# Performance work log

Hardware: AMD Instinct MI355X
Metric: run time of the kernel (lower is better)

## Reference

```python
import jax, jax.numpy as jnp
import numpy as np

NUM_EMBEDDINGS = 1024
EMBEDDING_DIM = 256
COMMITMENT_COST = 0.5
DECAY = 0.99
EPS = 1e-5


def setup_inputs() -> dict:
    key = jax.random.key(0)
    k1, k2, k3 = jax.random.split(key, 3)
    B, K, D = 64, 512, EMBEDDING_DIM
    return {
        "z_e": jax.random.normal(k1, (B, K, D), dtype=jnp.float32),
        "codebook": jax.random.normal(k2, (NUM_EMBEDDINGS, D), dtype=jnp.float32),
        "ema_cluster_size": jnp.ones((NUM_EMBEDDINGS,), dtype=jnp.float32),
        "ema_embed_sum": jax.random.normal(k3, (NUM_EMBEDDINGS, D), dtype=jnp.float32),
    }


def reference(z_e, codebook, ema_cluster_size, ema_embed_sum):
    B, K, D = z_e.shape
    flat = z_e.reshape(-1, D)  # [N, D]
    z_sq = jnp.sum(flat * flat, axis=1, keepdims=True)          # [N, 1]
    c_sq = jnp.sum(codebook * codebook, axis=1)[None, :]        # [1, E]
    distances = z_sq + c_sq - 2.0 * flat @ codebook.T           # [N, E]
    indices = jnp.argmin(distances, axis=1)                     # [N]
    z_q_flat = codebook[indices]                                # [N, D] gather (old codebook)

    # EMA statistics (training path), via segment sums instead of dense one-hot
    batch_cluster_size = jax.ops.segment_sum(
        jnp.ones_like(indices, dtype=flat.dtype), indices, num_segments=NUM_EMBEDDINGS)
    batch_embed_sum = jax.ops.segment_sum(flat, indices, num_segments=NUM_EMBEDDINGS)
    new_cluster_size = DECAY * ema_cluster_size + (1.0 - DECAY) * batch_cluster_size
    new_embed_sum = DECAY * ema_embed_sum + (1.0 - DECAY) * batch_embed_sum
    n = jnp.sum(new_cluster_size)
    smoothed = (new_cluster_size + EPS) / (n + NUM_EMBEDDINGS * EPS) * n
    new_codebook = new_embed_sum / smoothed[:, None]

    z_q = z_q_flat.reshape(B, K, D)
    commitment_loss = jnp.mean((z_e - jax.lax.stop_gradient(z_q)) ** 2)
    vq_loss = COMMITMENT_COST * commitment_loss
    # straight-through estimator
    z_q = z_e + jax.lax.stop_gradient(z_q - z_e)
    return z_q, vq_loss, indices.reshape(B, K), new_codebook, new_cluster_size, new_embed_sum
```

## Files before the change

kernel.cpp:

```cpp
#include <hip/hip_runtime.h>

typedef unsigned long long u64;
typedef unsigned int u32;
typedef __attribute__((ext_vector_type(8))) short short8;
typedef __attribute__((ext_vector_type(4))) float f32x4;

#define N_ROWS 32768
#define DIM    256
#define NE     1024

#define O_ZQ   0
#define O_LOSS 8388608
#define O_IDX  8388609
#define O_NCB  8421377
#define O_NCS  8683521
#define O_NES  8684545

#define OFF_LOSS   0
#define OFF_N      1
#define OFF_CSQ    64
#define OFF_CNT    1088
#define OFF_FILL   2112
#define OFF_BASE   3200
#define OFF_IDX    4224
#define OFF_BUCKET 36992
#define OFF_KEY    69888
#define OFF_CB16   135424

#define MARGIN   2.0f
#define LIST_CAP 3072

__device__ __forceinline__ unsigned short bf16rne(float x) {
    u32 b = __float_as_uint(x);
    return (unsigned short)((b + 0x7FFFu + ((b >> 16) & 1u)) >> 16);
}

__global__ __launch_bounds__(256) void prep_kernel(const float* __restrict__ cb,
                                                   float* __restrict__ ws,
                                                   float* __restrict__ out_nes) {
    const int tid = threadIdx.x, b = blockIdx.x;
    const int g = b * 256 + tid;

#pragma unroll
    for (int j = 0; j < 4; ++j) out_nes[g + j * 65536] = 0.f;
    if (g < N_ROWS) ((u64*)(ws + OFF_KEY))[g] = ~0ull;
    if (g < 2048) ws[OFF_CNT + g] = 0.f;
    if (g == 0) ws[OFF_LOSS] = 0.f;

    const int e = b * 4 + (tid >> 6);
    const int lane = tid & 63;
    float4 v = *(const float4*)(cb + (size_t)e * DIM + lane * 4);
    ushort4 h;
    h.x = bf16rne(v.x); h.y = bf16rne(v.y); h.z = bf16rne(v.z); h.w = bf16rne(v.w);
    *(ushort4*)((unsigned short*)(ws + OFF_CB16) + (size_t)e * DIM + lane * 4) = h;
    float s = v.x * v.x + v.y * v.y + v.z * v.z + v.w * v.w;
#pragma unroll
    for (int off = 32; off >= 1; off >>= 1) s += __shfl_down(s, off, 64);
    if (lane == 0) ws[OFF_CSQ + e] = s;
}

__global__ __launch_bounds__(512, 2) void vq_main(const float* __restrict__ z,
                                                  const float* __restrict__ cb,
                                                  float* __restrict__ ws,
                                                  float* __restrict__ out_zq,
                                                  float* __restrict__ out_idx) {
    __shared__ unsigned short zs[128][256];
    __shared__ unsigned short cbs[256][128];
    __shared__ float csq_s[NE];
    __shared__ u32   list[LIST_CAP];
    __shared__ int   lcnt;
    __shared__ int   sidx[128];
    __shared__ float lred[8];

    const int tid  = threadIdx.x;
    const int row0 = blockIdx.x * 128;
    const unsigned short* cb16 = (const unsigned short*)(ws + OFF_CB16);
    u64* keys = (u64*)(ws + OFF_KEY);

    if (tid == 0) lcnt = 0;
    csq_s[tid]       = ws[OFF_CSQ + tid];
    csq_s[tid + 512] = ws[OFF_CSQ + tid + 512];

#pragma unroll
    for (int sweep = 0; sweep < 8; ++sweep) {
        int fi = sweep * 4096 + tid * 8;
        int r = fi >> 8, c = fi & 255;
        const float4* src = (const float4*)(z + (size_t)row0 * DIM + fi);
        float4 v0 = src[0], v1 = src[1];
        short8 p;
        p[0] = (short)bf16rne(v0.x); p[1] = (short)bf16rne(v0.y);
        p[2] = (short)bf16rne(v0.z); p[3] = (short)bf16rne(v0.w);
        p[4] = (short)bf16rne(v1.x); p[5] = (short)bf16rne(v1.y);
        p[6] = (short)bf16rne(v1.z); p[7] = (short)bf16rne(v1.w);
        *(short8*)&zs[r][c ^ (8 * (r & 15))] = p;
    }

    const int wid = tid >> 6, lane = tid & 63;
    const int wm = wid >> 2, wn = wid & 3;
    const int l15 = lane & 15, l4 = lane >> 4;
    const int arow_base = wm * 64;
    const int swz = 8 * l15;

    float runmin[4][4];
#pragma unroll
    for (int m = 0; m < 4; ++m)
#pragma unroll
        for (int rg = 0; rg < 4; ++rg) runmin[m][rg] = 3.4e38f;

    for (int chunk = 0; chunk < 4; ++chunk) {
        const int e0 = chunk * 256;
        f32x4 acc[4][4];
#pragma unroll
        for (int m = 0; m < 4; ++m)
#pragma unroll
            for (int n = 0; n < 4; ++n) acc[m][n] = (f32x4){0.f, 0.f, 0.f, 0.f};

        for (int kh = 0; kh < 2; ++kh) {
            __syncthreads();
#pragma unroll
            for (int sweep = 0; sweep < 8; ++sweep) {
                int r  = sweep * 32 + (tid >> 4);
                int lk = (tid & 15) * 8;
                short8 v = *(const short8*)(cb16 + (size_t)(e0 + r) * DIM + kh * 128 + lk);
                *(short8*)&cbs[r][lk ^ (8 * (r & 15))] = v;
            }
            __syncthreads();
#pragma unroll
            for (int ks = 0; ks < 4; ++ks) {
                short8 a[4], bfr[4];
                int acol = kh * 128 + ks * 32 + 8 * l4;
                int bcol = ks * 32 + 8 * l4;
#pragma unroll
                for (int m = 0; m < 4; ++m)
                    a[m] = *(const short8*)&zs[arow_base + m * 16 + l15][acol ^ swz];
#pragma unroll
                for (int n = 0; n < 4; ++n)
                    bfr[n] = *(const short8*)&cbs[wn * 64 + n * 16 + l15][bcol ^ swz];
#pragma unroll
                for (int m = 0; m < 4; ++m)
#pragma unroll
                    for (int n = 0; n < 4; ++n)
                        acc[m][n] = __builtin_amdgcn_mfma_f32_16x16x32_bf16(
                            a[m], bfr[n], acc[m][n], 0, 0, 0);
            }
        }
        float cq[4];
#pragma unroll
        for (int n = 0; n < 4; ++n) cq[n] = csq_s[e0 + wn * 64 + n * 16 + l15];
#pragma unroll
        for (int m = 0; m < 4; ++m) {
#pragma unroll
            for (int rg = 0; rg < 4; ++rg) {
                float cmin = 3.4e38f;
#pragma unroll
                for (int n = 0; n < 4; ++n)
                    cmin = fminf(cmin, fmaf(-2.0f, acc[m][n][rg], cq[n]));
#pragma unroll
                for (int off = 1; off <= 8; off <<= 1)
                    cmin = fminf(cmin, __shfl_xor(cmin, off, 16));
                runmin[m][rg] = fminf(runmin[m][rg], cmin);
                float thr = runmin[m][rg] + MARGIN;
                int lrow = arow_base + m * 16 + l4 * 4 + rg;
#pragma unroll
                for (int n = 0; n < 4; ++n) {
                    float d = fmaf(-2.0f, acc[m][n][rg], cq[n]);
                    if (d <= thr) {
                        int slot = atomicAdd(&lcnt, 1);
                        if (slot < LIST_CAP)
                            list[slot] = ((u32)lrow << 10) |
                                         (u32)(e0 + wn * 64 + n * 16 + l15);
                    }
                }
            }
        }
    }
    __syncthreads();

    int nlist = lcnt < LIST_CAP ? lcnt : LIST_CAP;
    const int grp = tid >> 4, gl = tid & 15;
    for (int i = grp; i < nlist; i += 32) {
        u32 ent = list[i];
        int lrow = ent >> 10, code = ent & 1023;
        const float* zr = z + (size_t)(row0 + lrow) * DIM + gl * 16;
        const float* cr = cb + (size_t)code * DIM + gl * 16;
        float s = 0.f;
#pragma unroll
        for (int j = 0; j < 4; ++j) {
            float4 zv = ((const float4*)zr)[j];
            float4 cv = ((const float4*)cr)[j];
            s = fmaf(zv.x, cv.x, s); s = fmaf(zv.y, cv.y, s);
            s = fmaf(zv.z, cv.z, s); s = fmaf(zv.w, cv.w, s);
        }
#pragma unroll
        for (int off = 1; off <= 8; off <<= 1) s += __shfl_xor(s, off, 16);
        if (gl == 0) {
            float d = fmaf(-2.0f, s, csq_s[code]);
            u32 bb = __float_as_uint(d);
            u32 mm = (bb & 0x80000000u) ? ~bb : (bb | 0x80000000u);
            u64 key = ((u64)mm << 10) | (u32)code;
            atomicMin(&keys[row0 + lrow], key);
        }
    }
    __syncthreads();

    if (tid < 128) {
        u64 key = atomicMin(&keys[row0 + tid], ~0ull);
        int idx = (int)(key & 1023u);
        sidx[tid] = idx;
        out_idx[row0 + tid] = (float)idx;
        ((int*)ws)[OFF_IDX + row0 + tid] = idx;
        atomicAdd(&ws[OFF_CNT + idx], 1.0f);
    }
    __syncthreads();

    float lsum = 0.f;
    {
        int r = tid >> 2, part = tid & 3;
        int e = sidx[r];
        const float4* crow = (const float4*)(cb + (size_t)e * DIM + part * 64);
        const float4* zrow = (const float4*)(z + (size_t)(row0 + r) * DIM + part * 64);
        float4*       qrow = (float4*)(out_zq + (size_t)(row0 + r) * DIM + part * 64);
#pragma unroll
        for (int j = 0; j < 16; ++j) {
            float4 c4 = crow[j];
            float4 z4 = zrow[j];
            qrow[j] = c4;
            float dx = z4.x - c4.x, dy = z4.y - c4.y;
            float dz = z4.z - c4.z, dw = z4.w - c4.w;
            lsum += dx * dx + dy * dy + dz * dz + dw * dw;
        }
    }
#pragma unroll
    for (int off = 32; off >= 1; off >>= 1) lsum += __shfl_down(lsum, off, 64);
    if ((tid & 63) == 0) lred[tid >> 6] = lsum;
    __syncthreads();
    if (tid == 0) {
        float t = 0.f;
#pragma unroll
        for (int w = 0; w < 8; ++w) t += lred[w];
        atomicAdd(&ws[OFF_LOSS], t);
    }
}

__global__ __launch_bounds__(1024) void finalize_a(const float* __restrict__ ema_cs,
                                                   float* __restrict__ ws,
                                                   float* __restrict__ out_ncs,
                                                   float* __restrict__ out_loss) {
    __shared__ float wred[16];
    __shared__ int   wscan[16];
    const int tid = threadIdx.x, lane = tid & 63, w = tid >> 6;

    float cnt = ws[OFF_CNT + tid];
    float ncs = 0.99f * ema_cs[tid] + 0.01f * cnt;
    out_ncs[tid] = ncs;

    float s = ncs;
#pragma unroll
    for (int off = 32; off >= 1; off >>= 1) s += __shfl_down(s, off, 64);

    int v = (int)cnt;
    int x = v;
#pragma unroll
    for (int off = 1; off < 64; off <<= 1) {
        int o = __shfl_up(x, off, 64);
        if (lane >= off) x += o;
    }
    if (lane == 63) wscan[w] = x;
    if (lane == 0)  wred[w]  = s;
    __syncthreads();
    if (tid == 0) {
        float n = 0.f;
#pragma unroll
        for (int k = 0; k < 16; ++k) n += wred[k];
        ws[OFF_N] = n;
        out_loss[0] = 0.5f * ws[OFF_LOSS] / 8388608.0f;
        int run = 0;
#pragma unroll
        for (int k = 0; k < 16; ++k) { int t = wscan[k]; wscan[k] = run; run += t; }
    }
    __syncthreads();
    ((int*)ws)[OFF_BASE + tid] = x - v + wscan[w];
}

__global__ __launch_bounds__(256) void scatter_rows(float* __restrict__ ws) {
    int row = blockIdx.x * 256 + threadIdx.x;
    int* wsi = (int*)ws;
    int e = wsi[OFF_IDX + row];
    int slot = atomicAdd(&wsi[OFF_FILL + e], 1);
    wsi[OFF_BUCKET + wsi[OFF_BASE + e] + slot] = row;
}

__global__ __launch_bounds__(256) void seg_reduce(const float* __restrict__ z,
                                                  const float* __restrict__ ws,
                                                  float* __restrict__ bsum) {
    __shared__ int srow[32];
    __shared__ int scode[32];
    const int tid = threadIdx.x;
    const int p0  = blockIdx.x * 32;
    const int* wsi = (const int*)ws;

    if (tid < 32) {
        int row = wsi[OFF_BUCKET + p0 + tid];
        srow[tid]  = row;
        scode[tid] = wsi[OFF_IDX + row];
    }
    __syncthreads();

    const int d = tid;
    float acc = 0.f;
    int prev = scode[0];
#pragma unroll 4
    for (int i = 0; i < 32; ++i) {
        int e = scode[i];
        if (e != prev) {
            atomicAdd(&bsum[(size_t)prev * DIM + d], acc);
            acc = 0.f;
            prev = e;
        }
        acc += z[(size_t)srow[i] * DIM + d];
    }
    atomicAdd(&bsum[(size_t)prev * DIM + d], acc);
}

__global__ __launch_bounds__(256) void finalize_b(const float* __restrict__ ema_sum,
                                                  const float* __restrict__ ws,
                                                  const float* __restrict__ out_ncs,
                                                  float* __restrict__ out_nes,
                                                  float* __restrict__ out_ncb) {
    const int e = blockIdx.x, d = threadIdx.x;
    const size_t i = (size_t)e * DIM + d;
    float bsum = out_nes[i];
    float nes  = 0.99f * ema_sum[i] + 0.01f * bsum;
    out_nes[i] = nes;
    float ncs = out_ncs[e];
    float n   = ws[OFF_N];
    float sm  = (ncs + 1e-5f) / (n + NE * 1e-5f) * n;
    out_ncb[i] = nes / sm;
}

extern "C" void kernel_launch(void* const* d_in, const int* in_sizes, int n_in,
                              void* d_out, int out_size, void* d_ws, size_t ws_size,
                              hipStream_t stream) {
    const float* z_e      = (const float*)d_in[0];
    const float* codebook = (const float*)d_in[1];
    const float* ema_cs   = (const float*)d_in[2];
    const float* ema_sum  = (const float*)d_in[3];
    float* out = (float*)d_out;
    float* ws  = (float*)d_ws;

    prep_kernel<<<256, 256, 0, stream>>>(codebook, ws, out + O_NES);

    vq_main<<<256, 512, 0, stream>>>(z_e, codebook, ws, out + O_ZQ, out + O_IDX);

    finalize_a<<<1, 1024, 0, stream>>>(ema_cs, ws, out + O_NCS, out + O_LOSS);

    scatter_rows<<<N_ROWS / 256, 256, 0, stream>>>(ws);

    seg_reduce<<<N_ROWS / 32, 256, 0, stream>>>(z_e, ws, out + O_NES);

    finalize_b<<<NE, 256, 0, stream>>>(ema_sum, ws, out + O_NCS,
                                       out + O_NES, out + O_NCB);
}
```

Before: 228.5 us.

## Prefetch codebook tiles, compute loss from distances, fuse post-processing into cooperative kernel

Several changes land at once. In the main VQ kernel, the next codebook tile is prefetched into registers while the current tile is being multiplied, and the refinement dot products now use 4 lanes per candidate instead of 16. The commitment loss is derived from the winning distance plus a per-row ||z||^2 computed during staging, which removes the reread of z and codebook. The z_q write, finalize_a, scatter, segment reduce and finalize_b are merged into one cooperative kernel with grid syncs, which removes several launches at the cost of grid-wide barriers and register pressure from the prefetch. Deriving the loss from distances also changes its numerics slightly, since it is clamped at zero.

```diff
diff --git a/kernel.cpp b/kernel.cpp
--- a/kernel.cpp
+++ b/kernel.cpp
@@ -1,4 +1,7 @@
 #include <hip/hip_runtime.h>
+#include <hip/hip_cooperative_groups.h>
+
+namespace cg = cooperative_groups;
 
 typedef unsigned long long u64;
 typedef unsigned int u32;
@@ -62,24 +65,33 @@
 __global__ __launch_bounds__(512, 2) void vq_main(const float* __restrict__ z,
                                                   const float* __restrict__ cb,
                                                   float* __restrict__ ws,
-                                                  float* __restrict__ out_zq,
                                                   float* __restrict__ out_idx) {
     __shared__ unsigned short zs[128][256];
     __shared__ unsigned short cbs[256][128];
     __shared__ float csq_s[NE];
     __shared__ u32   list[LIST_CAP];
     __shared__ int   lcnt;
-    __shared__ int   sidx[128];
+    __shared__ float zsq_s[128];
     __shared__ float lred[8];
 
     const int tid  = threadIdx.x;
     const int row0 = blockIdx.x * 128;
     const unsigned short* cb16 = (const unsigned short*)(ws + OFF_CB16);
     u64* keys = (u64*)(ws + OFF_KEY);
+    int* wsi  = (int*)ws;
+
+    const int sr_c = tid >> 4;
+    const int lk_c = (tid & 15) * 8;
+    short8 stg[8];
+#pragma unroll
+    for (int s = 0; s < 8; ++s)
+        stg[s] = *(const short8*)(cb16 + (size_t)(s * 32 + sr_c) * DIM + lk_c);
 
     if (tid == 0) lcnt = 0;
+    if (tid < 128) zsq_s[tid] = 0.f;
     csq_s[tid]       = ws[OFF_CSQ + tid];
     csq_s[tid + 512] = ws[OFF_CSQ + tid + 512];
+    __syncthreads();
 
 #pragma unroll
     for (int sweep = 0; sweep < 8; ++sweep) {
@@ -93,6 +105,9 @@
         p[4] = (short)bf16rne(v1.x); p[5] = (short)bf16rne(v1.y);
         p[6] = (short)bf16rne(v1.z); p[7] = (short)bf16rne(v1.w);
         *(short8*)&zs[r][c ^ (8 * (r & 15))] = p;
+        float sq = v0.x * v0.x + v0.y * v0.y + v0.z * v0.z + v0.w * v0.w
+                 + v1.x * v1.x + v1.y * v1.y + v1.z * v1.z + v1.w * v1.w;
+        atomicAdd(&zsq_s[r], sq);
     }
 
     const int wid = tid >> 6, lane = tid & 63;
@@ -107,68 +122,77 @@
 #pragma unroll
         for (int rg = 0; rg < 4; ++rg) runmin[m][rg] = 3.4e38f;
 
-    for (int chunk = 0; chunk < 4; ++chunk) {
-        const int e0 = chunk * 256;
-        f32x4 acc[4][4];
-#pragma unroll
-        for (int m = 0; m < 4; ++m)
-#pragma unroll
-            for (int n = 0; n < 4; ++n) acc[m][n] = (f32x4){0.f, 0.f, 0.f, 0.f};
-
-        for (int kh = 0; kh < 2; ++kh) {
-            __syncthreads();
-#pragma unroll
-            for (int sweep = 0; sweep < 8; ++sweep) {
-                int r  = sweep * 32 + (tid >> 4);
-                int lk = (tid & 15) * 8;
-                short8 v = *(const short8*)(cb16 + (size_t)(e0 + r) * DIM + kh * 128 + lk);
-                *(short8*)&cbs[r][lk ^ (8 * (r & 15))] = v;
-            }
-            __syncthreads();
-#pragma unroll
-            for (int ks = 0; ks < 4; ++ks) {
-                short8 a[4], bfr[4];
-                int acol = kh * 128 + ks * 32 + 8 * l4;
-                int bcol = ks * 32 + 8 * l4;
-#pragma unroll
-                for (int m = 0; m < 4; ++m)
-                    a[m] = *(const short8*)&zs[arow_base + m * 16 + l15][acol ^ swz];
+    f32x4 acc[4][4];
+
+    for (int phase = 0; phase < 8; ++phase) {
+        const int chunk = phase >> 1, kh = phase & 1;
+        const int e0 = chunk << 8;
+        if (kh == 0) {
+#pragma unroll
+            for (int m = 0; m < 4; ++m)
+#pragma unroll
+                for (int n = 0; n < 4; ++n) acc[m][n] = (f32x4){0.f, 0.f, 0.f, 0.f};
+        }
+        __syncthreads();
+#pragma unroll
+        for (int s = 0; s < 8; ++s) {
+            int r = s * 32 + sr_c;
+            *(short8*)&cbs[r][lk_c ^ (8 * (r & 15))] = stg[s];
+        }
+        __syncthreads();
+        if (phase < 7) {
+            int np = phase + 1;
+            int nbase = (np >> 1) * 256, nkh = np & 1;
+#pragma unroll
+            for (int s = 0; s < 8; ++s)
+                stg[s] = *(const short8*)(cb16 + (size_t)(nbase + s * 32 + sr_c) * DIM
+                                          + nkh * 128 + lk_c);
+        }
+#pragma unroll
+        for (int ks = 0; ks < 4; ++ks) {
+            short8 a[4], bfr[4];
+            int acol = kh * 128 + ks * 32 + 8 * l4;
+            int bcol = ks * 32 + 8 * l4;
+#pragma unroll
+            for (int m = 0; m < 4; ++m)
+                a[m] = *(const short8*)&zs[arow_base + m * 16 + l15][acol ^ swz];
+#pragma unroll
+            for (int n = 0; n < 4; ++n)
+                bfr[n] = *(const short8*)&cbs[wn * 64 + n * 16 + l15][bcol ^ swz];
+#pragma unroll
+            for (int m = 0; m < 4; ++m)
 #pragma unroll
                 for (int n = 0; n < 4; ++n)
-                    bfr[n] = *(const short8*)&cbs[wn * 64 + n * 16 + l15][bcol ^ swz];
-#pragma unroll
-                for (int m = 0; m < 4; ++m)
+                    acc[m][n] = __builtin_amdgcn_mfma_f32_16x16x32_bf16(
+                        a[m], bfr[n], acc[m][n], 0, 0, 0);
+        }
+        if (kh == 1) {
+            float cq[4];
+#pragma unroll
+            for (int n = 0; n < 4; ++n) cq[n] = csq_s[e0 + wn * 64 + n * 16 + l15];
+#pragma unroll
+            for (int m = 0; m < 4; ++m) {
+#pragma unroll
+                for (int rg = 0; rg < 4; ++rg) {
+                    float cmin = 3.4e38f;
 #pragma unroll
                     for (int n = 0; n < 4; ++n)
-                        acc[m][n] = __builtin_amdgcn_mfma_f32_16x16x32_bf16(
-                            a[m], bfr[n], acc[m][n], 0, 0, 0);
-            }
-        }
-        float cq[4];
-#pragma unroll
-        for (int n = 0; n < 4; ++n) cq[n] = csq_s[e0 + wn * 64 + n * 16 + l15];
-#pragma unroll
-        for (int m = 0; m < 4; ++m) {
-#pragma unroll
-            for (int rg = 0; rg < 4; ++rg) {
-                float cmin = 3.4e38f;
-#pragma unroll
-                for (int n = 0; n < 4; ++n)
-                    cmin = fminf(cmin, fmaf(-2.0f, acc[m][n][rg], cq[n]));
-#pragma unroll
-                for (int off = 1; off <= 8; off <<= 1)
-                    cmin = fminf(cmin, __shfl_xor(cmin, off, 16));
-                runmin[m][rg] = fminf(runmin[m][rg], cmin);
-                float thr = runmin[m][rg] + MARGIN;
-                int lrow = arow_base + m * 16 + l4 * 4 + rg;
-#pragma unroll
-                for (int n = 0; n < 4; ++n) {
-                    float d = fmaf(-2.0f, acc[m][n][rg], cq[n]);
-                    if (d <= thr) {
-                        int slot = atomicAdd(&lcnt, 1);
-                        if (slot < LIST_CAP)
-                            list[slot] = ((u32)lrow << 10) |
-                                         (u32)(e0 + wn * 64 + n * 16 + l15);
+                        cmin = fminf(cmin, fmaf(-2.0f, acc[m][n][rg], cq[n]));
+#pragma unroll
+                    for (int off = 1; off <= 8; off <<= 1)
+                        cmin = fminf(cmin, __shfl_xor(cmin, off, 16));
+                    runmin[m][rg] = fminf(runmin[m][rg], cmin);
+                    float thr = runmin[m][rg] + MARGIN;
+                    int lrow = arow_base + m * 16 + l4 * 4 + rg;
+#pragma unroll
+                    for (int n = 0; n < 4; ++n) {
+                        float d = fmaf(-2.0f, acc[m][n][rg], cq[n]);
+                        if (d <= thr) {
+                            int slot = atomicAdd(&lcnt, 1);
+                            if (slot < LIST_CAP)
+                                list[slot] = ((u32)lrow << 10) |
+                                             (u32)(e0 + wn * 64 + n * 16 + l15);
+                        }
                     }
                 }
             }
@@ -177,22 +201,22 @@
     __syncthreads();
 
     int nlist = lcnt < LIST_CAP ? lcnt : LIST_CAP;
-    const int grp = tid >> 4, gl = tid & 15;
-    for (int i = grp; i < nlist; i += 32) {
+    const int grp = tid >> 2, gl = tid & 3;
+    for (int i = grp; i < nlist; i += 128) {
         u32 ent = list[i];
         int lrow = ent >> 10, code = ent & 1023;
-        const float* zr = z + (size_t)(row0 + lrow) * DIM + gl * 16;
-        const float* cr = cb + (size_t)code * DIM + gl * 16;
+        const float4* zr = (const float4*)(z + (size_t)(row0 + lrow) * DIM);
+        const float4* cr = (const float4*)(cb + (size_t)code * DIM);
         float s = 0.f;
 #pragma unroll
-        for (int j = 0; j < 4; ++j) {
-            float4 zv = ((const float4*)zr)[j];
-            float4 cv = ((const float4*)cr)[j];
+        for (int j = 0; j < 16; ++j) {
+            float4 zv = zr[j * 4 + gl];
+            float4 cv = cr[j * 4 + gl];
             s = fmaf(zv.x, cv.x, s); s = fmaf(zv.y, cv.y, s);
             s = fmaf(zv.z, cv.z, s); s = fmaf(zv.w, cv.w, s);
         }
-#pragma unroll
-        for (int off = 1; off <= 8; off <<= 1) s += __shfl_xor(s, off, 16);
+        s += __shfl_xor(s, 1, 4);
+        s += __shfl_xor(s, 2, 4);
         if (gl == 0) {
             float d = fmaf(-2.0f, s, csq_s[code]);
             u32 bb = __float_as_uint(d);
@@ -203,32 +227,17 @@
     }
     __syncthreads();
 
+    float lsum = 0.f;
     if (tid < 128) {
         u64 key = atomicMin(&keys[row0 + tid], ~0ull);
         int idx = (int)(key & 1023u);
-        sidx[tid] = idx;
+        u32 mm = (u32)(key >> 10);
+        u32 bb = (mm & 0x80000000u) ? (mm & 0x7fffffffu) : ~mm;
+        float dist = __uint_as_float(bb);
+        lsum = fmaxf(dist + zsq_s[tid], 0.f);
         out_idx[row0 + tid] = (float)idx;
-        ((int*)ws)[OFF_IDX + row0 + tid] = idx;
+        wsi[OFF_IDX + row0 + tid] = idx;
         atomicAdd(&ws[OFF_CNT + idx], 1.0f);
-    }
-    __syncthreads();
-
-    float lsum = 0.f;
-    {
-        int r = tid >> 2, part = tid & 3;
-        int e = sidx[r];
-        const float4* crow = (const float4*)(cb + (size_t)e * DIM + part * 64);
-        const float4* zrow = (const float4*)(z + (size_t)(row0 + r) * DIM + part * 64);
-        float4*       qrow = (float4*)(out_zq + (size_t)(row0 + r) * DIM + part * 64);
-#pragma unroll
-        for (int j = 0; j < 16; ++j) {
-            float4 c4 = crow[j];
-            float4 z4 = zrow[j];
-            qrow[j] = c4;
-            float dx = z4.x - c4.x, dy = z4.y - c4.y;
-            float dz = z4.z - c4.z, dw = z4.w - c4.w;
-            lsum += dx * dx + dy * dy + dz * dz + dw * dw;
-        }
     }
 #pragma unroll
     for (int off = 32; off >= 1; off >>= 1) lsum += __shfl_down(lsum, off, 64);
@@ -242,100 +251,124 @@
     }
 }
 
-__global__ __launch_bounds__(1024) void finalize_a(const float* __restrict__ ema_cs,
+__global__ __launch_bounds__(512) void post_kernel(const float* __restrict__ z,
+                                                   const float* __restrict__ cb,
+                                                   const float* __restrict__ ema_cs,
+                                                   const float* __restrict__ ema_sum,
                                                    float* __restrict__ ws,
-                                                   float* __restrict__ out_ncs,
-                                                   float* __restrict__ out_loss) {
-    __shared__ float wred[16];
-    __shared__ int   wscan[16];
-    const int tid = threadIdx.x, lane = tid & 63, w = tid >> 6;
-
-    float cnt = ws[OFF_CNT + tid];
-    float ncs = 0.99f * ema_cs[tid] + 0.01f * cnt;
-    out_ncs[tid] = ncs;
-
-    float s = ncs;
-#pragma unroll
-    for (int off = 32; off >= 1; off >>= 1) s += __shfl_down(s, off, 64);
-
-    int v = (int)cnt;
-    int x = v;
-#pragma unroll
-    for (int off = 1; off < 64; off <<= 1) {
-        int o = __shfl_up(x, off, 64);
-        if (lane >= off) x += o;
-    }
-    if (lane == 63) wscan[w] = x;
-    if (lane == 0)  wred[w]  = s;
-    __syncthreads();
-    if (tid == 0) {
-        float n = 0.f;
-#pragma unroll
-        for (int k = 0; k < 16; ++k) n += wred[k];
-        ws[OFF_N] = n;
-        out_loss[0] = 0.5f * ws[OFF_LOSS] / 8388608.0f;
-        int run = 0;
-#pragma unroll
-        for (int k = 0; k < 16; ++k) { int t = wscan[k]; wscan[k] = run; run += t; }
-    }
-    __syncthreads();
-    ((int*)ws)[OFF_BASE + tid] = x - v + wscan[w];
-}
-
-__global__ __launch_bounds__(256) void scatter_rows(float* __restrict__ ws) {
-    int row = blockIdx.x * 256 + threadIdx.x;
+                                                   float* __restrict__ out) {
+    cg::grid_group grid = cg::this_grid();
+    __shared__ float wred[8];
+    __shared__ int   wscan[8];
+    __shared__ int   srow2[2][32];
+    __shared__ int   scode2[2][32];
+
+    const int tid = threadIdx.x, bid = blockIdx.x;
     int* wsi = (int*)ws;
-    int e = wsi[OFF_IDX + row];
-    int slot = atomicAdd(&wsi[OFF_FILL + e], 1);
-    wsi[OFF_BUCKET + wsi[OFF_BASE + e] + slot] = row;
-}
-
-__global__ __launch_bounds__(256) void seg_reduce(const float* __restrict__ z,
-                                                  const float* __restrict__ ws,
-                                                  float* __restrict__ bsum) {
-    __shared__ int srow[32];
-    __shared__ int scode[32];
-    const int tid = threadIdx.x;
-    const int p0  = blockIdx.x * 32;
-    const int* wsi = (const int*)ws;
-
-    if (tid < 32) {
-        int row = wsi[OFF_BUCKET + p0 + tid];
-        srow[tid]  = row;
-        scode[tid] = wsi[OFF_IDX + row];
-    }
-    __syncthreads();
-
-    const int d = tid;
-    float acc = 0.f;
-    int prev = scode[0];
+    float* bsum = out + O_NES;
+
+    {
+        int r = bid * 128 + (tid >> 2), part = tid & 3;
+        int e = wsi[OFF_IDX + r];
+        const float4* crow = (const float4*)(cb + (size_t)e * DIM) + part * 16;
+        float4*       qrow = (float4*)(out + O_ZQ + (size_t)r * DIM) + part * 16;
+#pragma unroll
+        for (int j = 0; j < 16; ++j) qrow[j] = crow[j];
+    }
+    grid.sync();
+
+    if (bid == 0) {
+        const int lane = tid & 63, w = tid >> 6;
+        float c0 = ws[OFF_CNT + 2 * tid], c1 = ws[OFF_CNT + 2 * tid + 1];
+        float ncs0 = 0.99f * ema_cs[2 * tid] + 0.01f * c0;
+        float ncs1 = 0.99f * ema_cs[2 * tid + 1] + 0.01f * c1;
+        out[O_NCS + 2 * tid] = ncs0;
+        out[O_NCS + 2 * tid + 1] = ncs1;
+
+        float s = ncs0 + ncs1;
+#pragma unroll
+        for (int off = 32; off >= 1; off >>= 1) s += __shfl_down(s, off, 64);
+
+        int pair = (int)c0 + (int)c1;
+        int x = pair;
+#pragma unroll
+        for (int off = 1; off < 64; off <<= 1) {
+            int o = __shfl_up(x, off, 64);
+            if (lane >= off) x += o;
+        }
+        if (lane == 63) wscan[w] = x;
+        if (lane == 0)  wred[w]  = s;
+        __syncthreads();
+        if (tid == 0) {
+            float n = 0.f;
+#pragma unroll
+            for (int k = 0; k < 8; ++k) n += wred[k];
+            ws[OFF_N] = n;
+            out[O_LOSS] = 0.5f * ws[OFF_LOSS] / 8388608.0f;
+            int run = 0;
+#pragma unroll
+            for (int k = 0; k < 8; ++k) { int t = wscan[k]; wscan[k] = run; run += t; }
+        }
+        __syncthreads();
+        int base_pair = x - pair + wscan[w];
+        wsi[OFF_BASE + 2 * tid]     = base_pair;
+        wsi[OFF_BASE + 2 * tid + 1] = base_pair + (int)c0;
+    }
+    grid.sync();
+
+    {
+        int g = bid * 512 + tid;
+        if (g < N_ROWS) {
+            int e = wsi[OFF_IDX + g];
+            int slot = atomicAdd(&wsi[OFF_FILL + e], 1);
+            wsi[OFF_BUCKET + wsi[OFF_BASE + e] + slot] = g;
+        }
+    }
+    grid.sync();
+
+#pragma unroll
+    for (int s = 0; s < 2; ++s) {
+        __syncthreads();
+        if (tid < 64) {
+            int sub = tid >> 5, i = tid & 31;
+            int ck = bid * 4 + s * 2 + sub;
+            int row = wsi[OFF_BUCKET + ck * 32 + i];
+            srow2[sub][i]  = row;
+            scode2[sub][i] = wsi[OFF_IDX + row];
+        }
+        __syncthreads();
+        int sub = tid >> 8, d = tid & 255;
+        float acc = 0.f;
+        int prev = scode2[sub][0];
 #pragma unroll 4
-    for (int i = 0; i < 32; ++i) {
-        int e = scode[i];
-        if (e != prev) {
-            atomicAdd(&bsum[(size_t)prev * DIM + d], acc);
-            acc = 0.f;
-            prev = e;
-        }
-        acc += z[(size_t)srow[i] * DIM + d];
-    }
-    atomicAdd(&bsum[(size_t)prev * DIM + d], acc);
-}
-
-__global__ __launch_bounds__(256) void finalize_b(const float* __restrict__ ema_sum,
-                                                  const float* __restrict__ ws,
-                                                  const float* __restrict__ out_ncs,
-                                                  float* __restrict__ out_nes,
-                                                  float* __restrict__ out_ncb) {
-    const int e = blockIdx.x, d = threadIdx.x;
-    const size_t i = (size_t)e * DIM + d;
-    float bsum = out_nes[i];
-    float nes  = 0.99f * ema_sum[i] + 0.01f * bsum;
-    out_nes[i] = nes;
-    float ncs = out_ncs[e];
-    float n   = ws[OFF_N];
-    float sm  = (ncs + 1e-5f) / (n + NE * 1e-5f) * n;
-    out_ncb[i] = nes / sm;
+        for (int i = 0; i < 32; ++i) {
+            int e = scode2[sub][i];
+            if (e != prev) {
+                atomicAdd(&bsum[(size_t)prev * DIM + d], acc);
+                acc = 0.f;
+                prev = e;
+            }
+            acc += z[(size_t)srow2[sub][i] * DIM + d];
+        }
+        atomicAdd(&bsum[(size_t)prev * DIM + d], acc);
+    }
+    grid.sync();
+
+    {
+        float n = ws[OFF_N];
+#pragma unroll
+        for (int s = 0; s < 2; ++s) {
+            int e = bid * 4 + s * 2 + (tid >> 8);
+            int d = tid & 255;
+            size_t i = (size_t)e * DIM + d;
+            float bs  = bsum[i];
+            float nes = 0.99f * ema_sum[i] + 0.01f * bs;
+            out[O_NES + i] = nes;
+            float ncs = out[O_NCS + e];
+            float sm  = (ncs + 1e-5f) / (n + NE * 1e-5f) * n;
+            out[O_NCB + i] = nes / sm;
+        }
+    }
 }
 
 extern "C" void kernel_launch(void* const* d_in, const int* in_sizes, int n_in,
@@ -350,14 +383,15 @@
 
     prep_kernel<<<256, 256, 0, stream>>>(codebook, ws, out + O_NES);
 
-    vq_main<<<256, 512, 0, stream>>>(z_e, codebook, ws, out + O_ZQ, out + O_IDX);
-
-    finalize_a<<<1, 1024, 0, stream>>>(ema_cs, ws, out + O_NCS, out + O_LOSS);
-
-    scatter_rows<<<N_ROWS / 256, 256, 0, stream>>>(ws);
-
-    seg_reduce<<<N_ROWS / 32, 256, 0, stream>>>(z_e, ws, out + O_NES);
-
-    finalize_b<<<NE, 256, 0, stream>>>(ema_sum, ws, out + O_NCS,
-                                       out + O_NES, out + O_NCB);
-}
+    vq_main<<<256, 512, 0, stream>>>(z_e, codebook, ws, out + O_IDX);
+
+    void* pargs[6];
+    pargs[0] = (void*)&z_e;
+    pargs[1] = (void*)&codebook;
+    pargs[2] = (void*)&ema_cs;
+    pargs[3] = (void*)&ema_sum;
+    pargs[4] = (void*)&ws;
+    pargs[5] = (void*)&out;
+    hipLaunchCooperativeKernel((const void*)post_kernel, dim3(256), dim3(512),
+                               pargs, 0, stream);
+}
```

Measured after the change: 351.8 us. 1.54x slower.
